# Kernel optimization log

Hardware: AMD Instinct MI355X
Metric: run time of the kernel (lower is better)

The kernel has to match this reference:

```python
import jax, jax.numpy as jnp
import numpy as np

PATCH = 16
LOSS_WEIGHT = 1.0


def setup_inputs() -> dict:
    key = jax.random.key(0)
    cls_score = jax.random.normal(key, (8, 19, 512, 512), dtype=jnp.float32)
    return {"cls_score": cls_score}


def reference(cls_score):
    # Faithful to NuclearLoss(patch_size=16, use_softmax=True, inverse=False,
    # reduction='mean').
    N, C, H, W = cls_score.shape
    p = PATCH
    ph, pw = H // p, W // p
    logits = jax.nn.softmax(cls_score, axis=1)  # softmax over channel dim
    # patchify: (N,C,H,W) -> (N*L, p*p, C) with L = ph*pw
    x = logits.reshape(N, C, ph, p, pw, p)
    x = jnp.einsum('nchpwq->nhwpqc', x)
    patches = x.reshape(N * ph * pw, p * p, C)  # (B, p^2, C)
    # Original: mats = sqrt(bmm(P^T, P)) elementwise, loss = -sum(trace(mat)).
    # Only the diagonal of P^T P is needed: diag_k = sum_i P[i,k]^2.
    diag = jnp.sum(patches * patches, axis=1)          # (B, C)
    loss = -jnp.sum(jnp.sqrt(diag))
    loss = loss / patches.shape[0]                      # reduction='mean'
    return LOSS_WEIGHT * loss
```

## Files before the change

### kernel.cpp

```cpp
#include <hip/hip_runtime.h>
#include <math.h>


#define CCH   19
#define WW    512
#define CHST  (512 * 512)
#define IMGST (CCH * CHST)

typedef float    f4 __attribute__((ext_vector_type(4)));
typedef _Float16 h4 __attribute__((ext_vector_type(4)));

__global__ __launch_bounds__(256, 8) void nuclear_strip_kernel(
    const float* __restrict__ in, float* __restrict__ ws) {
    __shared__ float lds[4][16][CCH];

    const int tid  = threadIdx.x;
    const int w    = tid >> 6;
    const int lane = tid & 63;
    const int b    = blockIdx.x;
    const int n    = b >> 8;
    const int rp   = b & 255;
    const int row  = rp * 2 + (w >> 1);
    const int half = w & 1;

    const float* p = in + (size_t)n * IMGST + (size_t)row * WW
                        + half * 256 + (lane << 2);

    h4 h[CCH];
    f4 s = {0.0f, 0.0f, 0.0f, 0.0f};
#pragma unroll
    for (int c = 0; c < CCH; ++c) {
        f4 x = *(const f4*)(p + (size_t)c * CHST);
        f4 e;
        e.x = __expf(x.x);
        e.y = __expf(x.y);
        e.z = __expf(x.z);
        e.w = __expf(x.w);
        s += e;
        h[c] = __builtin_convertvector(e, h4);
    }
    f4 inv;
    inv.x = 1.0f / s.x;
    inv.y = 1.0f / s.y;
    inv.z = 1.0f / s.z;
    inv.w = 1.0f / s.w;

    const int seg = lane >> 2;
#pragma unroll
    for (int c = 0; c < CCH; ++c) {
        const f4 e = __builtin_convertvector(h[c], f4);
        const f4 t = e * inv;
        float v = t.x * t.x + t.y * t.y + t.z * t.z + t.w * t.w;
        v += __shfl_down(v, 2, 4);
        v += __shfl_down(v, 1, 4);
        if ((lane & 3) == 0) lds[w][seg][c] = v;
    }
    __syncthreads();

    float* wsb = ws + (size_t)b * 608;
    for (int k = tid; k < 608; k += 256) {
        const int pc = k / CCH;
        const int c  = k - pc * CCH;
        const int hh = pc >> 4;
        const int pp = pc & 15;
        wsb[k] = lds[hh][pp][c] + lds[hh + 2][pp][c];
    }
}

__global__ __launch_bounds__(256) void nuclear_finish_kernel(
    const float* __restrict__ ws, float* __restrict__ out) {
    const int i = blockIdx.x * 256 + threadIdx.x;
    const int g = i / 608;
    const int s = i - g * 608;
    const float* p = ws + (size_t)g * 8 * 608 + s;
    float d = 0.0f;
#pragma unroll
    for (int j = 0; j < 8; ++j) d += p[j * 608];
    float v = sqrtf(d);

    v += __shfl_down(v, 32, 64);
    v += __shfl_down(v, 16, 64);
    v += __shfl_down(v, 8, 64);
    v += __shfl_down(v, 4, 64);
    v += __shfl_down(v, 2, 64);
    v += __shfl_down(v, 1, 64);

    __shared__ float wsum[4];
    if ((threadIdx.x & 63) == 0) wsum[threadIdx.x >> 6] = v;
    __syncthreads();
    if (threadIdx.x == 0) {
        const float t = wsum[0] + wsum[1] + wsum[2] + wsum[3];
        atomicAdd(out, t * (-1.0f / 8192.0f));
    }
}

extern "C" void kernel_launch(void* const* d_in, const int* in_sizes, int n_in,
                              void* d_out, int out_size, void* d_ws, size_t ws_size,
                              hipStream_t stream) {
    const float* in = (const float*)d_in[0];
    float* ws  = (float*)d_ws;
    float* out = (float*)d_out;

    hipMemsetAsync(out, 0, sizeof(float), stream);

    nuclear_strip_kernel<<<2048, 256, 0, stream>>>(in, ws);
    nuclear_finish_kernel<<<608, 256, 0, stream>>>(ws, out);
}
```

Measured before the change: 244.5 us.

## Stage input rows into LDS via global_load_lds and accumulate four rows per block

The strip kernel now copies each 19-channel image row directly from global memory into LDS with the async global_load_lds builtin, then runs the softmax and sum of squares out of LDS. Each block walks four rows and accumulates per-patch partials in registers, so the grid is halved and the finish kernel sums four partials instead of eight. The fp16 staging of exponentials is removed. In exchange, the row loop has no double buffering and uses two barriers per row, which serialises load and compute, and the large LDS footprint limits occupancy.

```diff
diff --git a/kernel.cpp b/kernel.cpp
--- a/kernel.cpp
+++ b/kernel.cpp
@@ -3,79 +3,86 @@
 
 
 #define CCH   19
-#define WW    512
 #define CHST  (512 * 512)
 #define IMGST (CCH * CHST)
 
-typedef float    f4 __attribute__((ext_vector_type(4)));
-typedef _Float16 h4 __attribute__((ext_vector_type(4)));
+typedef float f2 __attribute__((ext_vector_type(2)));
 
-__global__ __launch_bounds__(256, 8) void nuclear_strip_kernel(
+__global__ __launch_bounds__(256, 4) void nuclear_dma_kernel(
     const float* __restrict__ in, float* __restrict__ ws) {
-    __shared__ float lds[4][16][CCH];
+    __shared__ float lds[CCH * 512];
 
     const int tid  = threadIdx.x;
     const int w    = tid >> 6;
     const int lane = tid & 63;
     const int b    = blockIdx.x;
-    const int n    = b >> 8;
-    const int rp   = b & 255;
-    const int row  = rp * 2 + (w >> 1);
-    const int half = w & 1;
+    const int n    = b >> 7;
+    const int g    = b & 127;
+    const int row0 = g << 2;
 
-    const float* p = in + (size_t)n * IMGST + (size_t)row * WW
-                        + half * 256 + (lane << 2);
+    float part[CCH];
+#pragma unroll
+    for (int c = 0; c < CCH; ++c) part[c] = 0.0f;
 
-    h4 h[CCH];
-    f4 s = {0.0f, 0.0f, 0.0f, 0.0f};
+    for (int r = 0; r < 4; ++r) {
+        const float* rowbase = in + (size_t)n * IMGST + (size_t)(row0 + r) * 512;
+        for (int j = w; j < 2 * CCH; j += 4) {
+            const int c    = j >> 1;
+            const int half = j & 1;
+            const float* src = rowbase + (size_t)c * CHST + half * 256 + lane * 4;
+            const float* dst = &lds[c * 512 + half * 256];
+            __builtin_amdgcn_global_load_lds(
+                (const __attribute__((address_space(1))) unsigned int*)src,
+                (__attribute__((address_space(3))) unsigned int*)dst,
+                16, 0, 0);
+        }
+        __syncthreads();
+
+        const f2* L = (const f2*)lds;
+        f2 e[CCH];
+        f2 s = {0.0f, 0.0f};
 #pragma unroll
-    for (int c = 0; c < CCH; ++c) {
-        f4 x = *(const f4*)(p + (size_t)c * CHST);
-        f4 e;
-        e.x = __expf(x.x);
-        e.y = __expf(x.y);
-        e.z = __expf(x.z);
-        e.w = __expf(x.w);
-        s += e;
-        h[c] = __builtin_convertvector(e, h4);
+        for (int c = 0; c < CCH; ++c) {
+            const f2 x = L[c * 256 + tid];
+            f2 ev;
+            ev.x = __expf(x.x);
+            ev.y = __expf(x.y);
+            e[c] = ev;
+            s += ev;
+        }
+        f2 inv;
+        inv.x = 1.0f / s.x;
+        inv.y = 1.0f / s.y;
+
+#pragma unroll
+        for (int c = 0; c < CCH; ++c) {
+            const f2 t = e[c] * inv;
+            float v = t.x * t.x + t.y * t.y;
+            v += __shfl_down(v, 4, 8);
+            v += __shfl_down(v, 2, 8);
+            v += __shfl_down(v, 1, 8);
+            part[c] += v;
+        }
+        __syncthreads();
     }
-    f4 inv;
-    inv.x = 1.0f / s.x;
-    inv.y = 1.0f / s.y;
-    inv.z = 1.0f / s.z;
-    inv.w = 1.0f / s.w;
 
-    const int seg = lane >> 2;
+    if ((tid & 7) == 0) {
+        const int pcol = tid >> 3;
 #pragma unroll
-    for (int c = 0; c < CCH; ++c) {
-        const f4 e = __builtin_convertvector(h[c], f4);
-        const f4 t = e * inv;
-        float v = t.x * t.x + t.y * t.y + t.z * t.z + t.w * t.w;
-        v += __shfl_down(v, 2, 4);
-        v += __shfl_down(v, 1, 4);
-        if ((lane & 3) == 0) lds[w][seg][c] = v;
+        for (int c = 0; c < CCH; ++c) lds[pcol * CCH + c] = part[c];
     }
     __syncthreads();
-
     float* wsb = ws + (size_t)b * 608;
-    for (int k = tid; k < 608; k += 256) {
-        const int pc = k / CCH;
-        const int c  = k - pc * CCH;
-        const int hh = pc >> 4;
-        const int pp = pc & 15;
-        wsb[k] = lds[hh][pp][c] + lds[hh + 2][pp][c];
-    }
+    for (int k = tid; k < 608; k += 256) wsb[k] = lds[k];
 }
 
 __global__ __launch_bounds__(256) void nuclear_finish_kernel(
     const float* __restrict__ ws, float* __restrict__ out) {
-    const int i = blockIdx.x * 256 + threadIdx.x;
-    const int g = i / 608;
-    const int s = i - g * 608;
-    const float* p = ws + (size_t)g * 8 * 608 + s;
-    float d = 0.0f;
-#pragma unroll
-    for (int j = 0; j < 8; ++j) d += p[j * 608];
+    const int i   = blockIdx.x * 256 + threadIdx.x;
+    const int pr2 = i / 608;
+    const int s   = i - pr2 * 608;
+    const float* p = ws + (size_t)pr2 * 4 * 608 + s;
+    float d = p[0] + p[608] + p[1216] + p[1824];
     float v = sqrtf(d);
 
     v += __shfl_down(v, 32, 64);
@@ -103,6 +110,6 @@
 
     hipMemsetAsync(out, 0, sizeof(float), stream);
 
-    nuclear_strip_kernel<<<2048, 256, 0, stream>>>(in, ws);
+    nuclear_dma_kernel<<<1024, 256, 0, stream>>>(in, ws);
     nuclear_finish_kernel<<<608, 256, 0, stream>>>(ws, out);
 }
```

Result: faster. 234.2 us (-4.2%).
